# Kernel tuning notes

Hardware: AMD Instinct MI355X
Metric: run time of the kernel (lower is better)

Reference implementation:

```python
import jax, jax.numpy as jnp
import numpy as np

B, S, H_DIM = 2, 2048, 1024
N_HEADS, HEAD_DIM = 16, 64
EPS = 1e-6


def phi(x):
    return jax.nn.elu(x) + 1.0


def setup_inputs() -> dict:
    key = jax.random.key(0)
    ks = jax.random.split(key, 11)
    std = 0.02
    proj = N_HEADS * HEAD_DIM
    return {
        "query": jax.random.normal(ks[0], (B, S, H_DIM), dtype=jnp.float32),
        "key": jax.random.normal(ks[1], (B, S, H_DIM), dtype=jnp.float32),
        "value": jax.random.normal(ks[2], (B, S, H_DIM), dtype=jnp.float32),
        "Wq": jax.random.normal(ks[3], (proj, H_DIM), dtype=jnp.float32) * std,
        "bq": jnp.zeros((proj,), dtype=jnp.float32),
        "Wk": jax.random.normal(ks[4], (proj, H_DIM), dtype=jnp.float32) * std,
        "bk": jnp.zeros((proj,), dtype=jnp.float32),
        "Wv": jax.random.normal(ks[5], (proj, H_DIM), dtype=jnp.float32) * std,
        "bv": jnp.zeros((proj,), dtype=jnp.float32),
        "Wo": jax.random.normal(ks[6], (H_DIM, proj), dtype=jnp.float32) * std,
        "bo": jnp.zeros((H_DIM,), dtype=jnp.float32),
    }


def reference(query, key, value, Wq, bq, Wk, bk, Wv, bv, Wo, bo):
    b, s, _ = query.shape
    # QKV projections (torch nn.Linear: y = x @ W.T + b)
    q = query @ Wq.T + bq
    k = key @ Wk.T + bk
    v = value @ Wv.T + bv
    # (b, s, h*d) -> (b, h, s, d)
    def split_heads(t):
        return t.reshape(b, s, N_HEADS, HEAD_DIM).transpose(0, 2, 1, 3)
    q, k, v = split_heads(q), split_heads(k), split_heads(v)

    q_phi = phi(q)  # (b,h,s,d)
    k_phi = phi(k)

    # cumulative outer products: (b,h,s,d_k,d_v)
    kv = k_phi[..., :, None] * v[..., None, :]
    kv_cumsum = jnp.cumsum(kv, axis=2)
    k_phi_cumsum = jnp.cumsum(k_phi, axis=2)

    out_num = jnp.einsum('bhsd,bhsdj->bhsj', q_phi, kv_cumsum)
    out_den = jnp.einsum('bhsd,bhsd->bhs', q_phi, k_phi_cumsum)
    out = out_num / (out_den[..., None] + EPS)

    out = out.transpose(0, 2, 1, 3).reshape(b, s, N_HEADS * HEAD_DIM)
    return out @ Wo.T + bo
```

## Files before the change

### kernel.cpp

```cpp
#include <hip/hip_runtime.h>
#include <hip/hip_bf16.h>
#include <stdint.h>

typedef __bf16 bf16x8 __attribute__((ext_vector_type(8)));
typedef float  f32x4  __attribute__((ext_vector_type(4)));
typedef __hip_bfloat16 hbf16;

#define AS1 __attribute__((address_space(1)))
#define AS3 __attribute__((address_space(3)))

__device__ __forceinline__ void gload_lds16(const void* g, void* l) {
  __builtin_amdgcn_global_load_lds((const AS1 void*)g, (AS3 void*)l, 16, 0, 0);
}

__device__ __forceinline__ f32x4 mfma_bf16(bf16x8 a, bf16x8 b, f32x4 c) {
  return __builtin_amdgcn_mfma_f32_16x16x32_bf16(a, b, c, 0, 0, 0);
}


__global__ __launch_bounds__(256) void convert_all(
    const float* __restrict__ q, const float* __restrict__ k, const float* __restrict__ v,
    const float* __restrict__ wq, const float* __restrict__ wk,
    const float* __restrict__ wv, const float* __restrict__ wo,
    hbf16* __restrict__ dst)
{
  const int i8 = (blockIdx.x * 256 + threadIdx.x) * 8;
  const float* src;
  int off;
  if      (i8 < (4  << 20)) { src = q;  off = i8; }
  else if (i8 < (8  << 20)) { src = k;  off = i8 - (4  << 20); }
  else if (i8 < (12 << 20)) { src = v;  off = i8 - (8  << 20); }
  else if (i8 < (13 << 20)) { src = wq; off = i8 - (12 << 20); }
  else if (i8 < (14 << 20)) { src = wk; off = i8 - (13 << 20); }
  else if (i8 < (15 << 20)) { src = wv; off = i8 - (14 << 20); }
  else                      { src = wo; off = i8 - (15 << 20); }
  const float4 a = *(const float4*)(src + off);
  const float4 b = *(const float4*)(src + off + 4);
  hbf16 h[8];
  h[0] = __float2bfloat16(a.x); h[1] = __float2bfloat16(a.y);
  h[2] = __float2bfloat16(a.z); h[3] = __float2bfloat16(a.w);
  h[4] = __float2bfloat16(b.x); h[5] = __float2bfloat16(b.y);
  h[6] = __float2bfloat16(b.z); h[7] = __float2bfloat16(b.w);
  *(uint4*)(dst + i8) = *(uint4*)h;
}

__device__ __forceinline__ void gemm_core_128(
    const hbf16* __restrict__ A, const hbf16* __restrict__ Bw,
    int by, int bx, hbf16* sA, hbf16* sB, f32x4 (&acc)[4][4])
{
  const int tid  = threadIdx.x;
  const int lane = tid & 63;
  const int wid  = tid >> 6;
  const int wm = wid >> 1, wn = wid & 1;
  const int l15 = lane & 15, l4 = lane >> 4;
  const int K = 1024;

  auto STAGE = [&](int kt) {
    const int k0 = kt * 64;
    #pragma unroll
    for (int j = 0; j < 4; ++j) {
      const int o   = (j * 256 + tid) * 16;
      const int row = o >> 7;
      const int csw = (o & 127) ^ ((row & 7) << 4);
      gload_lds16((const char*)A  + ((size_t)(by * 128 + row) * K + k0) * 2 + csw,
                  (char*)sA + o);
      gload_lds16((const char*)Bw + ((size_t)(bx * 128 + row) * K + k0) * 2 + csw,
                  (char*)sB + o);
    }
  };

  STAGE(0);
  for (int kt = 0; kt < 16; ++kt) {
    __syncthreads();
    bf16x8 af[2][4], bfr[2][4];
    #pragma unroll
    for (int kk = 0; kk < 2; ++kk) {
      #pragma unroll
      for (int m = 0; m < 4; ++m) {
        const int row = wm * 64 + m * 16 + l15;
        const int col = (kk * 64 + l4 * 16) ^ ((row & 7) << 4);
        af[kk][m] = *(const bf16x8*)((const char*)sA + row * 128 + col);
      }
      #pragma unroll
      for (int n = 0; n < 4; ++n) {
        const int row = wn * 64 + n * 16 + l15;
        const int col = (kk * 64 + l4 * 16) ^ ((row & 7) << 4);
        bfr[kk][n] = *(const bf16x8*)((const char*)sB + row * 128 + col);
      }
    }
    __syncthreads();
    if (kt < 15) STAGE(kt + 1);
    __builtin_amdgcn_sched_barrier(0);
    #pragma unroll
    for (int kk = 0; kk < 2; ++kk)
      #pragma unroll
      for (int m = 0; m < 4; ++m)
        #pragma unroll
        for (int n = 0; n < 4; ++n)
          acc[m][n] = mfma_bf16(af[kk][m], bfr[kk][n], acc[m][n]);
  }
}

__device__ __forceinline__ void xcd_remap(int& bx, int& by) {
  const int X = blockIdx.x, Y = blockIdx.y;
  by = X * 4 + (Y & 3);
  bx = Y >> 2;
}

__global__ __launch_bounds__(256, 3) void qkv_gemm(
    const hbf16* __restrict__ qin, const hbf16* __restrict__ kin, const hbf16* __restrict__ vin,
    const hbf16* __restrict__ wq, const hbf16* __restrict__ wk, const hbf16* __restrict__ wv,
    const float* __restrict__ bq, const float* __restrict__ bk, const float* __restrict__ bv,
    hbf16* __restrict__ q_phi, hbf16* __restrict__ k_phi,
    hbf16* __restrict__ kphiT, hbf16* __restrict__ vT)
{
  const int z = blockIdx.z;
  const hbf16* A    = (z == 0) ? qin : (z == 1) ? kin : vin;
  const hbf16* W    = (z == 0) ? wq  : (z == 1) ? wk  : wv;
  const float* bias = (z == 0) ? bq  : (z == 1) ? bk  : bv;

  int bx, by;
  xcd_remap(bx, by);

  __shared__ hbf16 smem[2 * 128 * 64];
  f32x4 acc[4][4] = {};
  gemm_core_128(A, W, by, bx, smem, smem + 128 * 64, acc);

  const int tid = threadIdx.x, lane = tid & 63, wid = tid >> 6;
  const int wm = wid >> 1, wn = wid & 1, l15 = lane & 15, l4 = lane >> 4;
  const int b = by >> 4;

  float bs[4];
  #pragma unroll
  for (int n = 0; n < 4; ++n) bs[n] = bias[bx * 128 + wn * 64 + n * 16 + l15];

  auto finish = [&](float v) -> float {
    return (z < 2) ? ((v > 0.f) ? (v + 1.f) : __expf(v)) : v;
  };

  if (z < 2) {
    #pragma unroll
    for (int n = 0; n < 4; ++n) {
      const int col = wn * 64 + n * 16 + l15;
      #pragma unroll
      for (int m = 0; m < 4; ++m) {
        #pragma unroll
        for (int j = 0; j < 4; ++j) {
          const int row = wm * 64 + m * 16 + l4 * 4 + j;
          smem[row * 128 + (col ^ ((row & 7) << 3))] =
              __float2bfloat16(finish(acc[m][n][j] + bs[n]));
        }
      }
    }
    __syncthreads();
    hbf16* dst = (z == 0) ? q_phi : k_phi;
    #pragma unroll
    for (int it = 0; it < 8; ++it) {
      const int sgi = it * 256 + tid;
      const int sl = sgi >> 4, seg = sgi & 15;
      const uint4 vv = *(const uint4*)&smem[sl * 128 + ((seg * 8) ^ ((sl & 7) << 3))];
      const int gnb = bx * 128 + seg * 8;
      const int h = gnb >> 6, dd = gnb & 63;
      const int s = (by * 128 + sl) & 2047;
      *(uint4*)&dst[(((size_t)(b * 16 + h)) * 2048 + s) * 64 + dd] = vv;
    }
  }
  if (z >= 1) {
    if (z == 1) __syncthreads();
    #pragma unroll
    for (int n = 0; n < 4; ++n) {
      const int gnl = wn * 64 + n * 16 + l15;
      const int x = (gnl & 7) << 3;
      #pragma unroll
      for (int m = 0; m < 4; ++m) {
        const int s0 = wm * 64 + m * 16 + l4 * 4;
        hbf16 pk[4];
        #pragma unroll
        for (int j = 0; j < 4; ++j)
          pk[j] = __float2bfloat16(finish(acc[m][n][j] + bs[n]));
        *(ushort4*)&smem[gnl * 128 + (s0 ^ x)] = *(ushort4*)pk;
      }
    }
    __syncthreads();
    hbf16* dst = (z == 1) ? kphiT : vT;
    #pragma unroll
    for (int it = 0; it < 8; ++it) {
      const int sgi = it * 256 + tid;
      const int gn = sgi >> 4, sseg = sgi & 15;
      const uint4 vv = *(const uint4*)&smem[gn * 128 + ((sseg * 8) ^ ((gn & 7) << 3))];
      const int gnb = bx * 128 + gn;
      const int h = gnb >> 6, dd = gnb & 63;
      const int sg = by * 128 + sseg * 8;
      const int c = (sg & 2047) >> 6, sin = sg & 63;
      *(uint4*)&dst[(((size_t)(b * 16 + h)) * 32 + c) * 4096 + dd * 64 + sin] = vv;
    }
  }
}

__global__ __launch_bounds__(256) void chunk_sums(
    const hbf16* __restrict__ kphiT, const hbf16* __restrict__ vT,
    float* __restrict__ sums)
{
  const int c = blockIdx.x, bh = blockIdx.y;
  const int tid = threadIdx.x, lane = tid & 63, w = tid >> 6;
  const int l15 = lane & 15, l4 = lane >> 4;
  const size_t tbase = ((size_t)bh * 32 + c) * 4096;

  f32x4 acc[5] = {};
  #pragma unroll
  for (int kk = 0; kk < 2; ++kk) {
    const bf16x8 bfr = *(const bf16x8*)&kphiT[tbase + (w * 16 + l15) * 64 + l4 * 8 + kk * 32];
    #pragma unroll
    for (int mj = 0; mj < 5; ++mj) {
      bf16x8 af;
      if (mj < 4) {
        af = *(const bf16x8*)&vT[tbase + (mj * 16 + l15) * 64 + l4 * 8 + kk * 32];
      } else {
        const __bf16 e = (l15 == 0) ? (__bf16)1.0f : (__bf16)0.0f;
        #pragma unroll
        for (int i = 0; i < 8; ++i) af[i] = e;
      }
      acc[mj] = mfma_bf16(af, bfr, acc[mj]);
    }
  }
  float* outp = sums + ((size_t)bh * 32 + c) * 5120;
  #pragma unroll
  for (int mj = 0; mj < 5; ++mj) {
    #pragma unroll
    for (int j = 0; j < 4; ++j) {
      outp[(mj * 16 + l4 * 4 + j) * 64 + w * 16 + l15] = acc[mj][j];
    }
  }
}

__global__ __launch_bounds__(256) void chunk_scan(
    const float* __restrict__ sums, hbf16* __restrict__ pre)
{
  const int elem = blockIdx.x * 256 + threadIdx.x;
  const int bh = blockIdx.y;
  const size_t base = (size_t)bh * 32 * 5120 + elem;
  float v[32];
  #pragma unroll
  for (int c = 0; c < 32; ++c) v[c] = sums[base + (size_t)c * 5120];
  float run = 0.f;
  #pragma unroll
  for (int c = 0; c < 32; ++c) {
    pre[base + (size_t)c * 5120] = __float2bfloat16(run);
    run += v[c];
  }
}

__global__ __launch_bounds__(256) void attn_chunk(
    const hbf16* __restrict__ q_phi, const hbf16* __restrict__ k_phi,
    const hbf16* __restrict__ vT, const hbf16* __restrict__ pre,
    hbf16* __restrict__ attn)
{
  const int c = blockIdx.x, bh = blockIdx.y;
  const int tid = threadIdx.x, lane = tid & 63, w = tid >> 6;
  const int l15 = lane & 15, l4 = lane >> 4;
  __shared__ hbf16 sS[4 * 16 * 64];

  const size_t qbase = ((size_t)bh * 2048 + c * 64) * 64;
  const size_t tbase = ((size_t)bh * 32 + c) * 4096;
  const size_t pbase = ((size_t)bh * 32 + c) * 5120;

  bf16x8 aq[2];
  #pragma unroll
  for (int kk = 0; kk < 2; ++kk)
    aq[kk] = *(const bf16x8*)&q_phi[qbase + (w * 16 + l15) * 64 + l4 * 8 + kk * 32];

  f32x4 accS[4] = {};
  #pragma unroll
  for (int kk = 0; kk < 2; ++kk) {
    #pragma unroll
    for (int ni = 0; ni < 4; ++ni) {
      const bf16x8 bk = *(const bf16x8*)&k_phi[qbase + (ni * 16 + l15) * 64 + l4 * 8 + kk * 32];
      accS[ni] = mfma_bf16(aq[kk], bk, accS[ni]);
    }
  }
  #pragma unroll
  for (int ni = 0; ni < 4; ++ni) {
    #pragma unroll
    for (int j = 0; j < 4; ++j) {
      const int r  = l4 * 4 + j;
      const int cc = ni * 16 + l15;
      const float v = (cc <= w * 16 + r) ? accS[ni][j] : 0.f;
      sS[w * 1024 + r * 64 + (cc ^ ((r & 7) << 3))] = __float2bfloat16(v);
    }
  }

  f32x4 accN[5] = {};
  #pragma unroll
  for (int kk = 0; kk < 2; ++kk) {
    const bf16x8 aS = *(const bf16x8*)&sS[w * 1024 + l15 * 64 +
                                          ((l4 * 8 + kk * 32) ^ ((l15 & 7) << 3))];
    #pragma unroll
    for (int ni = 0; ni < 5; ++ni) {
      bf16x8 bv;
      if (ni < 4) {
        bv = *(const bf16x8*)&vT[tbase + (ni * 16 + l15) * 64 + l4 * 8 + kk * 32];
      } else {
        const __bf16 e = (l15 == 0) ? (__bf16)1.0f : (__bf16)0.0f;
        #pragma unroll
        for (int i = 0; i < 8; ++i) bv[i] = e;
      }
      accN[ni] = mfma_bf16(aS, bv, accN[ni]);
    }
  }
  #pragma unroll
  for (int kk = 0; kk < 2; ++kk) {
    #pragma unroll
    for (int ni = 0; ni < 5; ++ni) {
      const bf16x8 bp = *(const bf16x8*)&pre[pbase + (ni * 16 + l15) * 64 + l4 * 8 + kk * 32];
      accN[ni] = mfma_bf16(aq[kk], bp, accN[ni]);
    }
  }
  const int b = bh >> 4, h = bh & 15;
  #pragma unroll
  for (int j = 0; j < 4; ++j) {
    const float den = __shfl(accN[4][j], lane & 48);
    const float inv = 1.f / (den + 1e-6f);
    const int sl = w * 16 + l4 * 4 + j;
    #pragma unroll
    for (int ni = 0; ni < 4; ++ni) {
      sS[sl * 64 + ((ni * 16 + l15) ^ ((sl & 7) << 3))] =
          __float2bfloat16(accN[ni][j] * inv);
    }
  }
  __syncthreads();
  #pragma unroll
  for (int it = 0; it < 2; ++it) {
    const int sgi = it * 256 + tid;
    const int sl = sgi >> 3, seg = sgi & 7;
    const uint4 vv = *(const uint4*)&sS[sl * 64 + ((seg * 8) ^ ((sl & 7) << 3))];
    *(uint4*)&attn[((size_t)b * 2048 + c * 64 + sl) * 1024 + h * 64 + seg * 8] = vv;
  }
}

__global__ __launch_bounds__(256, 3) void out_gemm(
    const hbf16* __restrict__ attn, const hbf16* __restrict__ wo,
    const float* __restrict__ bo, float* __restrict__ out)
{
  const int X = blockIdx.x, Y = blockIdx.y;
  const int by = X * 8 + (Y & 7);
  const int bx = Y >> 3;

  __shared__ hbf16 sA[64 * 64];
  __shared__ hbf16 sB[128 * 64];
  const int tid  = threadIdx.x;
  const int lane = tid & 63;
  const int wid  = tid >> 6;
  const int l15 = lane & 15, l4 = lane >> 4;
  const int K = 1024;

  auto STAGE = [&](int kt) {
    const int k0 = kt * 64;
    #pragma unroll
    for (int j = 0; j < 2; ++j) {
      const int o   = (j * 256 + tid) * 16;
      const int row = o >> 7;
      const int csw = (o & 127) ^ ((row & 7) << 4);
      gload_lds16((const char*)attn + ((size_t)(by * 64 + row) * K + k0) * 2 + csw,
                  (char*)sA + o);
    }
    #pragma unroll
    for (int j = 0; j < 4; ++j) {
      const int o   = (j * 256 + tid) * 16;
      const int row = o >> 7;
      const int csw = (o & 127) ^ ((row & 7) << 4);
      gload_lds16((const char*)wo + ((size_t)(bx * 128 + row) * K + k0) * 2 + csw,
                  (char*)sB + o);
    }
  };

  f32x4 acc[4][2] = {};
  STAGE(0);
  for (int kt = 0; kt < 16; ++kt) {
    __syncthreads();
    bf16x8 af[2][4], bfr[2][2];
    #pragma unroll
    for (int kk = 0; kk < 2; ++kk) {
      #pragma unroll
      for (int m = 0; m < 4; ++m) {
        const int row = m * 16 + l15;
        const int col = (kk * 64 + l4 * 16) ^ ((row & 7) << 4);
        af[kk][m] = *(const bf16x8*)((const char*)sA + row * 128 + col);
      }
      #pragma unroll
      for (int n = 0; n < 2; ++n) {
        const int row = wid * 32 + n * 16 + l15;
        const int col = (kk * 64 + l4 * 16) ^ ((row & 7) << 4);
        bfr[kk][n] = *(const bf16x8*)((const char*)sB + row * 128 + col);
      }
    }
    __syncthreads();
    if (kt < 15) STAGE(kt + 1);
    __builtin_amdgcn_sched_barrier(0);
    #pragma unroll
    for (int kk = 0; kk < 2; ++kk)
      #pragma unroll
      for (int m = 0; m < 4; ++m)
        #pragma unroll
        for (int n = 0; n < 2; ++n)
          acc[m][n] = mfma_bf16(af[kk][m], bfr[kk][n], acc[m][n]);
  }

  #pragma unroll
  for (int n = 0; n < 2; ++n) {
    const int gn = bx * 128 + wid * 32 + n * 16 + l15;
    const float bs = bo[gn];
    #pragma unroll
    for (int m = 0; m < 4; ++m) {
      #pragma unroll
      for (int j = 0; j < 4; ++j) {
        const int gm = by * 64 + m * 16 + l4 * 4 + j;
        out[(size_t)gm * 1024 + gn] = acc[m][n][j] + bs;
      }
    }
  }
}

extern "C" void kernel_launch(void* const* d_in, const int* in_sizes, int n_in,
                              void* d_out, int out_size, void* d_ws, size_t ws_size,
                              hipStream_t stream) {
  const float* q  = (const float*)d_in[0];
  const float* k  = (const float*)d_in[1];
  const float* v  = (const float*)d_in[2];
  const float* Wq = (const float*)d_in[3];
  const float* bq = (const float*)d_in[4];
  const float* Wk = (const float*)d_in[5];
  const float* bk = (const float*)d_in[6];
  const float* Wv = (const float*)d_in[7];
  const float* bv = (const float*)d_in[8];
  const float* Wo = (const float*)d_in[9];
  const float* bo = (const float*)d_in[10];

  char* ws = (char*)d_ws;
  const size_t MB = (size_t)1 << 20;
  hbf16* qin  = (hbf16*)(ws + 0 * MB);
  hbf16* kin  = (hbf16*)(ws + 8 * MB);
  hbf16* vin  = (hbf16*)(ws + 16 * MB);
  hbf16* wqb  = (hbf16*)(ws + 24 * MB);
  hbf16* wkb  = (hbf16*)(ws + 26 * MB);
  hbf16* wvb  = (hbf16*)(ws + 28 * MB);
  hbf16* wob  = (hbf16*)(ws + 30 * MB);
  hbf16* qphi = (hbf16*)(ws + 32 * MB);
  hbf16* kphi = (hbf16*)(ws + 40 * MB);
  hbf16* kphT = (hbf16*)(ws + 48 * MB);
  hbf16* vTb  = (hbf16*)(ws + 56 * MB);
  hbf16* attn = (hbf16*)(ws + 64 * MB);
  float* sums = (float*)(ws + 72 * MB);
  hbf16* pre  = (hbf16*)(ws + 92 * MB);

  convert_all<<<8192, 256, 0, stream>>>(q, k, v, Wq, Wk, Wv, Wo, qin);
  qkv_gemm<<<dim3(8, 32, 3), 256, 0, stream>>>(qin, kin, vin, wqb, wkb, wvb,
                                               bq, bk, bv, qphi, kphi, kphT, vTb);
  chunk_sums<<<dim3(32, 32), 256, 0, stream>>>(kphT, vTb, sums);
  chunk_scan<<<dim3(20, 32), 256, 0, stream>>>(sums, pre);
  attn_chunk<<<dim3(32, 32), 256, 0, stream>>>(qphi, kphi, vTb, pre, attn);
  out_gemm<<<dim3(8, 64), 256, 0, stream>>>(attn, wob, bo, (float*)d_out);
}
```

Baseline: 193.2 us.

## Fuse fp32-to-bf16 activation conversion into QKV GEMM A-tile loads

The separate conversion pass over the q/k/v activations is removed. The QKV GEMM now loads fp32 A tiles into registers, converts them to bf16 and writes them swizzled into LDS, while the weights still go through the global-to-LDS async path. This avoids writing and re-reading a bf16 copy of the activations, at the cost of twice the global A traffic per GEMM tile and extra register pressure from the prefetch buffers.

```diff
diff --git a/kernel.cpp b/kernel.cpp
--- a/kernel.cpp
+++ b/kernel.cpp
@@ -18,8 +18,7 @@
 }
 
 
-__global__ __launch_bounds__(256) void convert_all(
-    const float* __restrict__ q, const float* __restrict__ k, const float* __restrict__ v,
+__global__ __launch_bounds__(256) void convert_w(
     const float* __restrict__ wq, const float* __restrict__ wk,
     const float* __restrict__ wv, const float* __restrict__ wo,
     hbf16* __restrict__ dst)
@@ -27,13 +26,10 @@
   const int i8 = (blockIdx.x * 256 + threadIdx.x) * 8;
   const float* src;
   int off;
-  if      (i8 < (4  << 20)) { src = q;  off = i8; }
-  else if (i8 < (8  << 20)) { src = k;  off = i8 - (4  << 20); }
-  else if (i8 < (12 << 20)) { src = v;  off = i8 - (8  << 20); }
-  else if (i8 < (13 << 20)) { src = wq; off = i8 - (12 << 20); }
-  else if (i8 < (14 << 20)) { src = wk; off = i8 - (13 << 20); }
-  else if (i8 < (15 << 20)) { src = wv; off = i8 - (14 << 20); }
-  else                      { src = wo; off = i8 - (15 << 20); }
+  if      (i8 < (1 << 20)) { src = wq; off = i8; }
+  else if (i8 < (2 << 20)) { src = wk; off = i8 - (1 << 20); }
+  else if (i8 < (3 << 20)) { src = wv; off = i8 - (2 << 20); }
+  else                     { src = wo; off = i8 - (3 << 20); }
   const float4 a = *(const float4*)(src + off);
   const float4 b = *(const float4*)(src + off + 4);
   hbf16 h[8];
@@ -44,10 +40,31 @@
   *(uint4*)(dst + i8) = *(uint4*)h;
 }
 
-__device__ __forceinline__ void gemm_core_128(
-    const hbf16* __restrict__ A, const hbf16* __restrict__ Bw,
-    int by, int bx, hbf16* sA, hbf16* sB, f32x4 (&acc)[4][4])
-{
+__device__ __forceinline__ void xcd_remap(int& bx, int& by) {
+  const int X = blockIdx.x, Y = blockIdx.y;
+  by = X * 4 + (Y & 3);
+  bx = Y >> 2;
+}
+
+__global__ __launch_bounds__(256, 3) void qkv_gemm(
+    const float* __restrict__ qin, const float* __restrict__ kin, const float* __restrict__ vin,
+    const hbf16* __restrict__ wq, const hbf16* __restrict__ wk, const hbf16* __restrict__ wv,
+    const float* __restrict__ bq, const float* __restrict__ bk, const float* __restrict__ bv,
+    hbf16* __restrict__ q_phi, hbf16* __restrict__ k_phi,
+    hbf16* __restrict__ kphiT, hbf16* __restrict__ vT)
+{
+  const int z = blockIdx.z;
+  const float* A32  = (z == 0) ? qin : (z == 1) ? kin : vin;
+  const hbf16* W    = (z == 0) ? wq  : (z == 1) ? wk  : wv;
+  const float* bias = (z == 0) ? bq  : (z == 1) ? bk  : bv;
+
+  int bx, by;
+  xcd_remap(bx, by);
+
+  __shared__ hbf16 smem[2 * 128 * 64];
+  hbf16* sA = smem;
+  hbf16* sB = smem + 128 * 64;
+
   const int tid  = threadIdx.x;
   const int lane = tid & 63;
   const int wid  = tid >> 6;
@@ -55,21 +72,50 @@
   const int l15 = lane & 15, l4 = lane >> 4;
   const int K = 1024;
 
-  auto STAGE = [&](int kt) {
+  auto STAGEB = [&](int kt) {
     const int k0 = kt * 64;
     #pragma unroll
     for (int j = 0; j < 4; ++j) {
       const int o   = (j * 256 + tid) * 16;
       const int row = o >> 7;
       const int csw = (o & 127) ^ ((row & 7) << 4);
-      gload_lds16((const char*)A  + ((size_t)(by * 128 + row) * K + k0) * 2 + csw,
-                  (char*)sA + o);
-      gload_lds16((const char*)Bw + ((size_t)(bx * 128 + row) * K + k0) * 2 + csw,
+      gload_lds16((const char*)W + ((size_t)(bx * 128 + row) * K + k0) * 2 + csw,
                   (char*)sB + o);
     }
   };
-
-  STAGE(0);
+  auto LOADA = [&](int kt, float4 (&av)[4][2]) {
+    #pragma unroll
+    for (int j = 0; j < 4; ++j) {
+      const int o   = (j * 256 + tid) * 16;
+      const int row = o >> 7;
+      const int col = (o & 127) >> 1;
+      const float4* src =
+          (const float4*)&A32[((size_t)(by * 128 + row)) * K + kt * 64 + col];
+      av[j][0] = src[0];
+      av[j][1] = src[1];
+    }
+  };
+  auto WRITEA = [&](float4 (&av)[4][2]) {
+    #pragma unroll
+    for (int j = 0; j < 4; ++j) {
+      const int o   = (j * 256 + tid) * 16;
+      const int row = o >> 7;
+      const int osw = (o & ~127) | ((o & 127) ^ ((row & 7) << 4));
+      const float* f = (const float*)av[j];
+      hbf16 h[8];
+      #pragma unroll
+      for (int i = 0; i < 8; ++i) h[i] = __float2bfloat16(f[i]);
+      *(uint4*)((char*)sA + osw) = *(uint4*)h;
+    }
+  };
+
+  f32x4 acc[4][4] = {};
+  float4 av[4][2];
+
+  STAGEB(0);
+  LOADA(0, av);
+  WRITEA(av);
+
   for (int kt = 0; kt < 16; ++kt) {
     __syncthreads();
     bf16x8 af[2][4], bfr[2][4];
@@ -89,7 +135,10 @@
       }
     }
     __syncthreads();
-    if (kt < 15) STAGE(kt + 1);
+    if (kt < 15) {
+      STAGEB(kt + 1);
+      LOADA(kt + 1, av);
+    }
     __builtin_amdgcn_sched_barrier(0);
     #pragma unroll
     for (int kk = 0; kk < 2; ++kk)
@@ -98,38 +147,11 @@
         #pragma unroll
         for (int n = 0; n < 4; ++n)
           acc[m][n] = mfma_bf16(af[kk][m], bfr[kk][n], acc[m][n]);
-  }
-}
-
-__device__ __forceinline__ void xcd_remap(int& bx, int& by) {
-  const int X = blockIdx.x, Y = blockIdx.y;
-  by = X * 4 + (Y & 3);
-  bx = Y >> 2;
-}
-
-__global__ __launch_bounds__(256, 3) void qkv_gemm(
-    const hbf16* __restrict__ qin, const hbf16* __restrict__ kin, const hbf16* __restrict__ vin,
-    const hbf16* __restrict__ wq, const hbf16* __restrict__ wk, const hbf16* __restrict__ wv,
-    const float* __restrict__ bq, const float* __restrict__ bk, const float* __restrict__ bv,
-    hbf16* __restrict__ q_phi, hbf16* __restrict__ k_phi,
-    hbf16* __restrict__ kphiT, hbf16* __restrict__ vT)
-{
-  const int z = blockIdx.z;
-  const hbf16* A    = (z == 0) ? qin : (z == 1) ? kin : vin;
-  const hbf16* W    = (z == 0) ? wq  : (z == 1) ? wk  : wv;
-  const float* bias = (z == 0) ? bq  : (z == 1) ? bk  : bv;
-
-  int bx, by;
-  xcd_remap(bx, by);
-
-  __shared__ hbf16 smem[2 * 128 * 64];
-  f32x4 acc[4][4] = {};
-  gemm_core_128(A, W, by, bx, smem, smem + 128 * 64, acc);
-
-  const int tid = threadIdx.x, lane = tid & 63, wid = tid >> 6;
-  const int wm = wid >> 1, wn = wid & 1, l15 = lane & 15, l4 = lane >> 4;
+    __builtin_amdgcn_sched_barrier(0);
+    if (kt < 15) WRITEA(av);
+  }
+
   const int b = by >> 4;
-
   float bs[4];
   #pragma unroll
   for (int n = 0; n < 4; ++n) bs[n] = bias[bx * 128 + wn * 64 + n * 16 + l15];
@@ -437,9 +459,6 @@
 
   char* ws = (char*)d_ws;
   const size_t MB = (size_t)1 << 20;
-  hbf16* qin  = (hbf16*)(ws + 0 * MB);
-  hbf16* kin  = (hbf16*)(ws + 8 * MB);
-  hbf16* vin  = (hbf16*)(ws + 16 * MB);
   hbf16* wqb  = (hbf16*)(ws + 24 * MB);
   hbf16* wkb  = (hbf16*)(ws + 26 * MB);
   hbf16* wvb  = (hbf16*)(ws + 28 * MB);
@@ -452,8 +471,8 @@
   float* sums = (float*)(ws + 72 * MB);
   hbf16* pre  = (hbf16*)(ws + 92 * MB);
 
-  convert_all<<<8192, 256, 0, stream>>>(q, k, v, Wq, Wk, Wv, Wo, qin);
-  qkv_gemm<<<dim3(8, 32, 3), 256, 0, stream>>>(qin, kin, vin, wqb, wkb, wvb,
+  convert_w<<<2048, 256, 0, stream>>>(Wq, Wk, Wv, Wo, wqb);
+  qkv_gemm<<<dim3(8, 32, 3), 256, 0, stream>>>(q, k, v, wqb, wkb, wvb,
                                                bq, bk, bv, qphi, kphi, kphT, vTb);
   chunk_sums<<<dim3(32, 32), 256, 0, stream>>>(kphT, vTb, sums);
   chunk_scan<<<dim3(20, 32), 256, 0, stream>>>(sums, pre);
```

Result: slower. 261.1 us (+35.1%).
